# Kernel tuning notes

Measured on AMD Instinct MI355X. Metric: run time of the kernel, lower is better.

## Reference

```python
import jax, jax.numpy as jnp
import numpy as np

DIM = 2048
N_HEADS = 32
HEAD_DIM = DIM // N_HEADS
D_FF = 4 * DIM
EPS = 1e-5


def layernorm(x, g, b):
    mu = jnp.mean(x, axis=-1, keepdims=True)
    var = jnp.mean(jnp.square(x - mu), axis=-1, keepdims=True)
    return (x - mu) * jax.lax.rsqrt(var + EPS) * g + b


def setup_inputs() -> dict:
    key = jax.random.key(0)
    ks = jax.random.split(key, 12)
    s = 0.02
    # Linear weights stored as [in, out] (y = x @ W + b), equivalent math to torch's x @ W.T
    return {
        "x": jax.random.normal(ks[0], (2, 2048, DIM), jnp.float32),
        "w_qkv": jax.random.normal(ks[1], (DIM, 3 * DIM), jnp.float32) * s,
        "b_qkv": jnp.zeros((3 * DIM,), jnp.float32),
        "w_o": jax.random.normal(ks[2], (DIM, DIM), jnp.float32) * s,
        "b_o": jnp.zeros((DIM,), jnp.float32),
        "g1": jnp.ones((DIM,), jnp.float32),
        "beta1": jnp.zeros((DIM,), jnp.float32),
        "w1": jax.random.normal(ks[3], (DIM, D_FF), jnp.float32) * s,
        "b1": jnp.zeros((D_FF,), jnp.float32),
        "w2": jax.random.normal(ks[4], (D_FF, DIM), jnp.float32) * s,
        "b2": jnp.zeros((DIM,), jnp.float32),
        "g2": jnp.ones((DIM,), jnp.float32),
        "beta2": jnp.zeros((DIM,), jnp.float32),
    }


def reference(x, w_qkv, b_qkv, w_o, b_o, g1, beta1, w1, b1, w2, b2, g2, beta2):
    B, T, _ = x.shape
    residual = x
    h = layernorm(x, g1, beta1)
    qkv = h @ w_qkv + b_qkv                      # [B,T,3*DIM]
    qkv = qkv.reshape(B, T, 3, N_HEADS, HEAD_DIM)
    qkv = jnp.transpose(qkv, (2, 0, 3, 1, 4))    # [3,B,H,T,D]
    q, k, v = qkv[0], qkv[1], qkv[2]
    scores = jnp.einsum("bhtd,bhsd->bhts", q, k) / np.sqrt(HEAD_DIM).astype(np.float32)
    attn = jax.nn.softmax(scores, axis=-1)       # full T x T (non-causal), as in source
    out = jnp.einsum("bhts,bhsd->bhtd", attn, v)
    out = jnp.transpose(out, (0, 2, 1, 3)).reshape(B, T, DIM)
    h = out @ w_o + b_o
    x = h + residual
    residual = x
    h = layernorm(x, g2, beta2)
    h = jax.nn.gelu(h @ w1 + b1, approximate=False)  # torch nn.GELU default = exact erf
    h = h @ w2 + b2
    return h + residual
```

## Files before the change

kernel.cpp:

```cpp
#include <hip/hip_runtime.h>
#include <hip/hip_bf16.h>

#define DIM  2048
#define DFF  8192
#define NH   32
#define HD   64
#define TT   2048
#define MM   4096

typedef __attribute__((ext_vector_type(4))) float f32x4;
typedef __attribute__((ext_vector_type(4))) unsigned int u32x4;
typedef __attribute__((ext_vector_type(2))) unsigned int u32x2;
typedef unsigned short ushort_t;

#define MFMA16(ACC, A, B) \
  asm volatile("v_mfma_f32_16x16x32_bf16 %0, %1, %2, %0" : "+v"(ACC) : "v"(A), "v"(B))
#define MFMA16A(ACC, A, B) \
  asm volatile("v_mfma_f32_16x16x32_bf16 %0, %1, %2, %0" : "+a"(ACC) : "v"(A), "v"(B))

#define GL16(GP, LP)                                                     \
  __builtin_amdgcn_global_load_lds(                                      \
      (const __attribute__((address_space(1))) void*)(GP),               \
      (__attribute__((address_space(3))) void*)(LP), 16, 0, 0)

#define VM(N) do{ asm volatile("s_waitcnt vmcnt(" #N ")");               \
                  __builtin_amdgcn_sched_barrier(0); }while(0)
#define NOOP  ((void)0)

template <int IMM>
__device__ __forceinline__ u32x4 dsr(unsigned a) {
  u32x4 d;
  asm volatile("ds_read_b128 %0, %1 offset:%2" : "=v"(d) : "v"(a), "i"(IMM));
  return d;
}

__device__ __forceinline__ unsigned int f2bu(float f) {
  union { __hip_bfloat16 h; unsigned short u; } c;
  c.h = __float2bfloat16(f);
  return (unsigned int)c.u;
}
__device__ __forceinline__ float fexp2(float x) {
  float r; asm("v_exp_f32 %0, %1" : "=v"(r) : "v"(x)); return r;
}
__device__ __forceinline__ unsigned cvtpk(float lo, float hi) {
  unsigned r; asm("v_cvt_pk_bf16_f32 %0, %1, %2" : "=v"(r) : "v"(lo), "v"(hi));
  return r;
}
__device__ __forceinline__ float fmax3(float a, float b, float c) {
  float r; asm("v_max3_f32 %0, %1, %2, %3" : "=v"(r) : "v"(a), "v"(b), "v"(c));
  return r;
}

__global__ __launch_bounds__(256)
void transpose_cvt(const float* __restrict__ in, __hip_bfloat16* __restrict__ out,
                   int R, int C) {
  __shared__ float tile[32][33];
  const int tx = threadIdx.x, ty = threadIdx.y;
  const int bx = blockIdx.x * 32, by = blockIdx.y * 32;
#pragma unroll
  for (int i = 0; i < 32; i += 8)
    tile[ty + i][tx] = in[(size_t)(by + ty + i) * C + bx + tx];
  __syncthreads();
#pragma unroll
  for (int i = 0; i < 32; i += 8)
    out[(size_t)(bx + ty + i) * R + by + tx] = __float2bfloat16(tile[tx][ty + i]);
}

__global__ __launch_bounds__(256)
void ln_kernel(const float* __restrict__ in, const float* __restrict__ gw,
               const float* __restrict__ bw, __hip_bfloat16* __restrict__ out) {
  const int row = blockIdx.x;
  const int t = threadIdx.x;
  const float* x = in + (size_t)row * DIM;
  const float4 v0 = ((const float4*)x)[t * 2];
  const float4 v1 = ((const float4*)x)[t * 2 + 1];
  float s  = v0.x + v0.y + v0.z + v0.w + v1.x + v1.y + v1.z + v1.w;
  float ss = v0.x*v0.x + v0.y*v0.y + v0.z*v0.z + v0.w*v0.w
           + v1.x*v1.x + v1.y*v1.y + v1.z*v1.z + v1.w*v1.w;
#pragma unroll
  for (int o = 32; o >= 1; o >>= 1) { s += __shfl_xor(s, o); ss += __shfl_xor(ss, o); }
  __shared__ float red[8];
  if ((t & 63) == 0) { red[t >> 6] = s; red[4 + (t >> 6)] = ss; }
  __syncthreads();
  s  = red[0] + red[1] + red[2] + red[3];
  ss = red[4] + red[5] + red[6] + red[7];
  const float mean = s * (1.0f / DIM);
  const float rstd = rsqrtf(ss * (1.0f / DIM) - mean * mean + 1e-5f);
  const float4 g0 = ((const float4*)gw)[t * 2], g1 = ((const float4*)gw)[t * 2 + 1];
  const float4 b0 = ((const float4*)bw)[t * 2], b1 = ((const float4*)bw)[t * 2 + 1];
  uint4 o;
  o.x = f2bu((v0.x - mean) * rstd * g0.x + b0.x) | (f2bu((v0.y - mean) * rstd * g0.y + b0.y) << 16);
  o.y = f2bu((v0.z - mean) * rstd * g0.z + b0.z) | (f2bu((v0.w - mean) * rstd * g0.w + b0.w) << 16);
  o.z = f2bu((v1.x - mean) * rstd * g1.x + b1.x) | (f2bu((v1.y - mean) * rstd * g1.y + b1.y) << 16);
  o.w = f2bu((v1.z - mean) * rstd * g1.z + b1.z) | (f2bu((v1.w - mean) * rstd * g1.w + b1.w) << 16);
  *(uint4*)((char*)out + ((size_t)row * DIM + t * 8) * 2) = o;
}

template <int EPI>
__global__ __launch_bounds__(512, 2)
void gemm256(const __hip_bfloat16* __restrict__ Abf, const __hip_bfloat16* __restrict__ Btbf,
             const float* __restrict__ bias, const float* __restrict__ res,
             void* __restrict__ o0, void* __restrict__ o1, void* __restrict__ o2,
             int M, int N, int K, int nkt) {
  __shared__ ushort_t lds[2][2][16384];
  const int tid = threadIdx.x;
  const int l = tid & 63, w = tid >> 6;
  const int wm = w >> 2, wn = w & 3;
  const int g = l >> 4, q15 = l & 15;

  const int nby = M >> 8;
  const int nwg = (N >> 8) * nby;
  int id = blockIdx.x;
  {
    const int qq = nwg >> 3, rr = nwg & 7;
    const int xcd = id & 7, pos = id >> 3;
    id = (xcd < rr ? xcd * (qq + 1) : rr * (qq + 1) + (xcd - rr) * qq) + pos;
  }
  const int bm = (id % nby) << 8;
  const int bn = (id / nby) << 8;
  const int k0 = (EPI == 4) ? (int)blockIdx.y * (nkt << 6) : 0;

  const ushort_t* Au = (const ushort_t*)Abf;
  const ushort_t* Bu = (const ushort_t*)Btbf;
  const int sr = tid >> 3;
  const int sc = (((tid & 7) ^ (sr & 7)) << 3);
  const ushort_t* aBase = Au + (size_t)(bm + sr) * K + (k0 + sc);
  const ushort_t* bBase = Bu + (size_t)(bn + sr) * K + (k0 + sc);
  const int dOff = (w << 9) + (l << 3);

#define SA(BUF, GRP, KT_)                                                \
  GL16(aBase + (size_t)((GRP) << 6) * K + ((KT_) << 6),                  \
       &lds[BUF][0][((GRP) << 12) + dOff])
#define SB(BUF, GRP, KT_)                                                \
  GL16(bBase + (size_t)((GRP) << 6) * K + ((KT_) << 6),                  \
       &lds[BUF][1][((GRP) << 12) + dOff])

  const unsigned lbase =
      (unsigned)(size_t)(__attribute__((address_space(3))) ushort_t*)&lds[0][0][0];
  const int x7 = q15 & 7;
  const unsigned laneA = (unsigned)(q15 * 128);
  const unsigned c0 = (unsigned)((g ^ x7) * 16);
  const unsigned c1 = (unsigned)(((4 | g) ^ x7) * 16);
  const unsigned aAk0b0 = lbase + wm * 8192 + laneA + c0;
  const unsigned aAk1b0 = lbase + wm * 8192 + laneA + c1;
  const unsigned aAk0b1 = aAk0b0 + 65536;
  const unsigned aAk1b1 = aAk1b0 + 65536;
  const unsigned aBk0b0 = lbase + 32768 + wn * 8192 + laneA + c0;
  const unsigned aBk1b0 = lbase + 32768 + wn * 8192 + laneA + c1;
  const unsigned aBk0b1 = aBk0b0 + 65536;
  const unsigned aBk1b1 = aBk1b0 + 65536;

#define AOFFC(M) (((M) & 4) * 4096 + ((M) & 3) * 2048)
#define RDA(BUF, M0, M1) do{                                             \
    af[0][0] = dsr<AOFFC(M0)>(aAk0b##BUF);                               \
    af[0][1] = dsr<AOFFC(M0)>(aAk1b##BUF);                               \
    af[1][0] = dsr<AOFFC(M1)>(aAk0b##BUF);                               \
    af[1][1] = dsr<AOFFC(M1)>(aAk1b##BUF); }while(0)
#define RDB(BUF) do{                                                     \
    bf[0][0] = dsr<0>(aBk0b##BUF);    bf[0][1] = dsr<0>(aBk1b##BUF);     \
    bf[1][0] = dsr<2048>(aBk0b##BUF); bf[1][1] = dsr<2048>(aBk1b##BUF);  \
    bf[2][0] = dsr<4096>(aBk0b##BUF); bf[2][1] = dsr<4096>(aBk1b##BUF);  \
    bf[3][0] = dsr<6144>(aBk0b##BUF); bf[3][1] = dsr<6144>(aBk1b##BUF); }while(0)

#define LGK0 do{ asm volatile("s_waitcnt lgkmcnt(0)");                   \
                 __builtin_amdgcn_sched_barrier(0); }while(0)

#define CLUSTER(R0, R1) do{                                              \
    __builtin_amdgcn_s_setprio(1);                                       \
    MFMA16A(acc[R0][0], af[0][0], bf[0][0]);                             \
    MFMA16A(acc[R0][1], af[0][0], bf[1][0]);                             \
    MFMA16A(acc[R0][2], af[0][0], bf[2][0]);                             \
    MFMA16A(acc[R0][3], af[0][0], bf[3][0]);                             \
    MFMA16A(acc[R1][0], af[1][0], bf[0][0]);                             \
    MFMA16A(acc[R1][1], af[1][0], bf[1][0]);                             \
    MFMA16A(acc[R1][2], af[1][0], bf[2][0]);                             \
    MFMA16A(acc[R1][3], af[1][0], bf[3][0]);                             \
    MFMA16A(acc[R0][0], af[0][1], bf[0][1]);                             \
    MFMA16A(acc[R0][1], af[0][1], bf[1][1]);                             \
    MFMA16A(acc[R0][2], af[0][1], bf[2][1]);                             \
    MFMA16A(acc[R0][3], af[0][1], bf[3][1]);                             \
    MFMA16A(acc[R1][0], af[1][1], bf[0][1]);                             \
    MFMA16A(acc[R1][1], af[1][1], bf[1][1]);                             \
    MFMA16A(acc[R1][2], af[1][1], bf[2][1]);                             \
    MFMA16A(acc[R1][3], af[1][1], bf[3][1]);                             \
    __builtin_amdgcn_s_setprio(0); }while(0)

#define HALF(BUF, OBUF, ktA23, PFA, ktN, PFN, W1C, W3C)                  \
  do {                                                                   \
    if (PFA) { SA(OBUF, 2, ktA23); SA(OBUF, 3, ktA23); }                 \
    RDB(BUF); RDA(BUF, 0, 1);                                            \
    __builtin_amdgcn_s_barrier();                                        \
    LGK0; CLUSTER(0, 1);                                                 \
    __builtin_amdgcn_s_barrier();                                        \
    if (PFN) { SB(BUF, 0, ktN); SB(BUF, 1, ktN); }                       \
    RDA(BUF, 2, 3);                                                      \
    __builtin_amdgcn_s_barrier();                                        \
    LGK0; CLUSTER(2, 3);                                                 \
    W1C;                                                                 \
    __builtin_amdgcn_s_barrier();                                        \
    if (PFN) { SB(BUF, 2, ktN); SB(BUF, 3, ktN); }                       \
    RDA(BUF, 4, 5);                                                      \
    __builtin_amdgcn_s_barrier();                                        \
    LGK0; CLUSTER(4, 5);                                                 \
    __builtin_amdgcn_s_barrier();                                        \
    if (PFN) { SA(BUF, 0, ktN); SA(BUF, 1, ktN); }                       \
    RDA(BUF, 6, 7);                                                      \
    __builtin_amdgcn_s_barrier();                                        \
    LGK0; CLUSTER(6, 7);                                                 \
    W3C;                                                                 \
    __builtin_amdgcn_s_barrier();                                        \
  } while (0)

  f32x4 acc[8][4];
#pragma unroll
  for (int a = 0; a < 8; ++a)
#pragma unroll
    for (int b = 0; b < 4; ++b) acc[a][b] = (f32x4)0.0f;

  u32x4 bf[4][2], af[2][2];

  SB(0, 0, 0); SB(0, 1, 0); SB(0, 2, 0); SB(0, 3, 0);
  SA(0, 0, 0); SA(0, 1, 0); SA(0, 2, 0); SA(0, 3, 0);
  SB(1, 0, 1); SB(1, 1, 1); SB(1, 2, 1); SB(1, 3, 1);
  SA(1, 0, 1); SA(1, 1, 1);
  VM(8);
  __builtin_amdgcn_s_barrier();

  int kt = 0;
  for (; kt + 3 < nkt; kt += 2) {
    HALF(0, 1, kt + 1, true, kt + 2, true, VM(10), VM(8));
    HALF(1, 0, kt + 2, true, kt + 3, true, VM(10), VM(8));
  }
  HALF(0, 1, kt + 1, true,  kt + 2, false, VM(8), VM(2));
  HALF(1, 0, kt + 2, false, kt + 3, false, VM(0), NOOP);

#pragma unroll
  for (int m = 0; m < 8; ++m) {
    const int row0 = bm + ((m & 4) << 5) + (wm << 6) + ((m & 3) << 4) + (g << 2);
#pragma unroll
    for (int n = 0; n < 4; ++n) {
      const int col = bn + (wn << 6) + (n << 4) + q15;
      float bv = 0.0f;
      if constexpr (EPI != 4) bv = bias[col];
#pragma unroll
      for (int i = 0; i < 4; ++i) {
        const int mrow = row0 + i;
        float v = acc[m][n][i] + bv;
        if constexpr (EPI == 0) {
          const int sel = col >> 11, hd = col & 2047, h = hd >> 6, d = hd & 63;
          const int b = mrow >> 11, t = mrow & 2047;
          if (sel == 0) {
            ((__hip_bfloat16*)o0)[((size_t)(b * NH + h) * TT + t) * HD + d] =
                __float2bfloat16(v * 0.18033688011112042f);
          } else if (sel == 1) {
            ((__hip_bfloat16*)o1)[((size_t)(b * NH + h) * TT + t) * HD + d] =
                __float2bfloat16(v);
          } else {
            ((__hip_bfloat16*)o2)[((size_t)(b * NH + h) * HD + d) * TT + t] =
                __float2bfloat16(v);
          }
        } else if constexpr (EPI == 2) {
          ((__hip_bfloat16*)o0)[(size_t)mrow * N + col] =
              __float2bfloat16(0.5f * v * (1.0f + erff(v * 0.70710678118654752f)));
        } else {
          ((float*)(blockIdx.y ? o1 : o0))[(size_t)mrow * N + col] = v;
        }
      }
    }
  }
#undef SA
#undef SB
#undef RDA
#undef RDB
#undef HALF
#undef CLUSTER
#undef LGK0
#undef AOFFC
}

__global__ __launch_bounds__(256)
void combine2(const float* __restrict__ p0, const float* __restrict__ p1,
              const float* __restrict__ bias, const float* __restrict__ res,
              float* __restrict__ out) {
  const size_t i = ((size_t)blockIdx.x * 256 + threadIdx.x) << 2;
  const float4 a = *(const float4*)(p0 + i);
  const float4 b = *(const float4*)(p1 + i);
  const float4 r = *(const float4*)(res + i);
  const float4 bi = *(const float4*)(bias + (i & (DIM - 1)));
  float4 o;
  o.x = a.x + b.x + r.x + bi.x;
  o.y = a.y + b.y + r.y + bi.y;
  o.z = a.z + b.z + r.z + bi.z;
  o.w = a.w + b.w + r.w + bi.w;
  *(float4*)(out + i) = o;
}

template <int EPI>
__global__ __launch_bounds__(256)
void gemm_bt(const __hip_bfloat16* __restrict__ A, const __hip_bfloat16* __restrict__ Bt,
             const float* __restrict__ bias, const float* __restrict__ res,
             void* __restrict__ o0, int M, int N, int K) {
  __shared__ __hip_bfloat16 As[128 * 32];
  __shared__ __hip_bfloat16 Bs[128 * 32];
  const int tid = threadIdx.x;
  const int l = tid & 63, w = tid >> 6;
  const int wr = w >> 1, wc = w & 1;
  const int g = l >> 4, q15 = l & 15;
  const int bm = blockIdx.y * 128, bn = blockIdx.x * 128;

  f32x4 acc[4][4];
#pragma unroll
  for (int a = 0; a < 4; ++a)
#pragma unroll
    for (int b = 0; b < 4; ++b) acc[a][b] = (f32x4)0.0f;

  const __hip_bfloat16* aSrc = A  + (size_t)(bm + (tid >> 2)) * K + (tid & 3) * 8;
  const __hip_bfloat16* bSrc = Bt + (size_t)(bn + (tid >> 2)) * K + (tid & 3) * 8;
  __hip_bfloat16* aDst = As + tid * 8;
  __hip_bfloat16* bDst = Bs + tid * 8;
  const size_t rowStep = (size_t)64 * K;

  for (int kt = 0; kt < K; kt += 32) {
    GL16(aSrc + kt,            aDst);
    GL16(aSrc + rowStep + kt,  aDst + 2048);
    GL16(bSrc + kt,            bDst);
    GL16(bSrc + rowStep + kt,  bDst + 2048);
    __syncthreads();
    u32x4 af[4], bf[4];
#pragma unroll
    for (int rb = 0; rb < 4; ++rb)
      af[rb] = *(const u32x4*)(As + (wr * 64 + rb * 16 + q15) * 32 + g * 8);
#pragma unroll
    for (int cb = 0; cb < 4; ++cb)
      bf[cb] = *(const u32x4*)(Bs + (wc * 64 + cb * 16 + q15) * 32 + g * 8);
#pragma unroll
    for (int rb = 0; rb < 4; ++rb)
#pragma unroll
      for (int cb = 0; cb < 4; ++cb) MFMA16(acc[rb][cb], af[rb], bf[cb]);
    __syncthreads();
  }

#pragma unroll
  for (int rb = 0; rb < 4; ++rb) {
    const int row0 = bm + wr * 64 + rb * 16 + g * 4;
#pragma unroll
    for (int cb = 0; cb < 4; ++cb) {
      const int col = bn + wc * 64 + cb * 16 + q15;
      const float bv = bias[col];
#pragma unroll
      for (int i = 0; i < 4; ++i) {
        const int m = row0 + i;
        float v = acc[rb][cb][i] + bv;
        ((float*)o0)[(size_t)m * N + col] = v + res[(size_t)m * N + col];
      }
    }
  }
}

__global__ __launch_bounds__(256)
void attn_kernel(const __hip_bfloat16* __restrict__ Q, const __hip_bfloat16* __restrict__ Kx,
                 const __hip_bfloat16* __restrict__ Vt, __hip_bfloat16* __restrict__ out) {
  __shared__ unsigned int Plds[4][2048];
  const int tid = threadIdx.x;
  const int l = tid & 63, w = tid >> 6;
  const int g = l >> 4, q15 = l & 15;
  const int bh = blockIdx.x >> 3;
  const int q0 = (blockIdx.x & 7) * 256 + w * 64;
  const __hip_bfloat16* Qb = Q  + (size_t)bh * TT * HD;
  const __hip_bfloat16* Kb = Kx + (size_t)bh * TT * HD;
  const __hip_bfloat16* Vb = Vt + (size_t)bh * HD * TT;
  unsigned int* Pw = Plds[w];

  u32x4 qf[4][2];
#pragma unroll
  for (int rb = 0; rb < 4; ++rb)
#pragma unroll
    for (int ks = 0; ks < 2; ++ks)
      qf[rb][ks] = *(const u32x4*)(Qb + (size_t)(q0 + rb * 16 + q15) * HD + ks * 32 + g * 8);

  f32x4 acc[4][4];
#pragma unroll
  for (int a = 0; a < 4; ++a)
#pragma unroll
    for (int b = 0; b < 4; ++b) acc[a][b] = (f32x4)0.0f;
  float mstat[4] = {-3e38f, -3e38f, -3e38f, -3e38f};
  float lstat[4] = {0.f, 0.f, 0.f, 0.f};

  u32x4 kf[2][4];
#pragma unroll
  for (int cb = 0; cb < 4; ++cb)
#pragma unroll
    for (int ks = 0; ks < 2; ++ks)
      kf[ks][cb] = *(const u32x4*)(Kb + (size_t)(cb * 16 + q15) * HD + ks * 32 + g * 8);

  for (int s0 = 0; s0 < TT; s0 += 64) {
    f32x4 st[4][4];
#pragma unroll
    for (int a = 0; a < 4; ++a)
#pragma unroll
      for (int b = 0; b < 4; ++b) st[a][b] = (f32x4)0.0f;
    __builtin_amdgcn_s_setprio(1);
#pragma unroll
    for (int ks = 0; ks < 2; ++ks)
#pragma unroll
      for (int cb = 0; cb < 4; ++cb)
#pragma unroll
        for (int rb = 0; rb < 4; ++rb) MFMA16(st[cb][rb], kf[ks][cb], qf[rb][ks]);
    __builtin_amdgcn_s_setprio(0);
    if (s0 + 64 < TT) {
#pragma unroll
      for (int cb = 0; cb < 4; ++cb)
#pragma unroll
        for (int ks = 0; ks < 2; ++ks)
          kf[ks][cb] = *(const u32x4*)(Kb + (size_t)(s0 + 64 + cb * 16 + q15) * HD + ks * 32 + g * 8);
    }
#pragma unroll
    for (int rb = 0; rb < 4; ++rb) {
      float a0 = fmax3(st[0][rb][0], st[0][rb][1], st[0][rb][2]);
      float a1 = fmax3(st[0][rb][3], st[1][rb][0], st[1][rb][1]);
      float a2 = fmax3(st[1][rb][2], st[1][rb][3], st[2][rb][0]);
      float a3 = fmax3(st[2][rb][1], st[2][rb][2], st[2][rb][3]);
      float a4 = fmax3(st[3][rb][0], st[3][rb][1], st[3][rb][2]);
      float pm = fmax3(fmax3(a0, a1, a2), a3, fmax3(a4, st[3][rb][3], a0));
      pm = fmaxf(pm, __shfl_xor(pm, 16));
      pm = fmaxf(pm, __shfl_xor(pm, 32));
      if (!__all(pm <= mstat[rb] + 8.0f)) {
        const float mnew = fmaxf(mstat[rb], pm);
        const float corr = fexp2(mstat[rb] - mnew);
        mstat[rb] = mnew;
        lstat[rb] *= corr;
#pragma unroll
        for (int db = 0; db < 4; ++db)
#pragma unroll
          for (int i = 0; i < 4; ++i) acc[db][rb][i] *= corr;
      }
      const float mcur = mstat[rb];
      float rs = 0.f;
      const int row = rb * 16 + q15;
      const int rx = row & 7;
#pragma unroll
      for (int cb = 0; cb < 4; ++cb) {
        const float p0 = fexp2(st[cb][rb][0] - mcur);
        const float p1 = fexp2(st[cb][rb][1] - mcur);
        const float p2 = fexp2(st[cb][rb][2] - mcur);
        const float p3 = fexp2(st[cb][rb][3] - mcur);
        rs += (p0 + p1) + (p2 + p3);
        const int seg = (cb * 2 + (g >> 1)) ^ rx;
        u32x2 pk = {cvtpk(p0, p1), cvtpk(p2, p3)};
        *(u32x2*)(Pw + row * 32 + seg * 4 + (g & 1) * 2) = pk;
      }
      rs += __shfl_xor(rs, 16);
      rs += __shfl_xor(rs, 32);
      lstat[rb] += rs;
    }
    u32x4 vf[2][4];
#pragma unroll
    for (int ks2 = 0; ks2 < 2; ++ks2)
#pragma unroll
      for (int db = 0; db < 4; ++db)
        vf[ks2][db] = *(const u32x4*)(Vb + (size_t)(db * 16 + q15) * TT + s0 + ks2 * 32 + g * 8);
    u32x4 pf[2][4];
#pragma unroll
    for (int ks2 = 0; ks2 < 2; ++ks2)
#pragma unroll
      for (int rb = 0; rb < 4; ++rb) {
        const int row = rb * 16 + q15;
        const int seg = (ks2 * 4 + g) ^ (row & 7);
        pf[ks2][rb] = *(const u32x4*)(Pw + row * 32 + seg * 4);
      }
    __builtin_amdgcn_s_setprio(1);
#pragma unroll
    for (int ks2 = 0; ks2 < 2; ++ks2)
#pragma unroll
      for (int db = 0; db < 4; ++db)
#pragma unroll
        for (int rb = 0; rb < 4; ++rb) MFMA16(acc[db][rb], vf[ks2][db], pf[ks2][rb]);
    __builtin_amdgcn_s_setprio(0);
  }
  const int b = bh >> 5, hh = bh & 31;
#pragma unroll
  for (int rb = 0; rb < 4; ++rb) {
    const float inv = 1.0f / lstat[rb];
    const size_t trow = (size_t)(b * TT + q0 + rb * 16 + q15);
#pragma unroll
    for (int db = 0; db < 4; ++db) {
      u32x2 pk = {cvtpk(acc[db][rb][0] * inv, acc[db][rb][1] * inv),
                  cvtpk(acc[db][rb][2] * inv, acc[db][rb][3] * inv)};
      *(u32x2*)(out + trow * DIM + hh * 64 + db * 16 + g * 4) = pk;
    }
  }
}

extern "C" void kernel_launch(void* const* d_in, const int* in_sizes, int n_in,
                              void* d_out, int out_size, void* d_ws, size_t ws_size,
                              hipStream_t stream) {
  (void)in_sizes; (void)n_in; (void)out_size; (void)ws_size;
  const float* x     = (const float*)d_in[0];
  const float* w_qkv = (const float*)d_in[1];
  const float* b_qkv = (const float*)d_in[2];
  const float* w_o   = (const float*)d_in[3];
  const float* b_o   = (const float*)d_in[4];
  const float* g1    = (const float*)d_in[5];
  const float* be1   = (const float*)d_in[6];
  const float* w1    = (const float*)d_in[7];
  const float* b1    = (const float*)d_in[8];
  const float* w2    = (const float*)d_in[9];
  const float* b2    = (const float*)d_in[10];
  const float* g2    = (const float*)d_in[11];
  const float* be2   = (const float*)d_in[12];

  char* ws = (char*)d_ws;
  size_t off = 0;
  auto alloc = [&](size_t bytes) {
    void* p = ws + off;
    off += (bytes + 255) & ~(size_t)255;
    return p;
  };
  __hip_bfloat16* WqkvT = (__hip_bfloat16*)alloc((size_t)6144 * 2048 * 2);
  __hip_bfloat16* WoT   = (__hip_bfloat16*)alloc((size_t)2048 * 2048 * 2);
  __hip_bfloat16* W1T   = (__hip_bfloat16*)alloc((size_t)8192 * 2048 * 2);
  __hip_bfloat16* W2T   = (__hip_bfloat16*)alloc((size_t)2048 * 8192 * 2);
  __hip_bfloat16* hbuf  = (__hip_bfloat16*)alloc((size_t)MM * DIM * 2);
  float*          xres  = (float*)alloc((size_t)MM * DIM * 4);
  __hip_bfloat16* Qb    = (__hip_bfloat16*)alloc((size_t)MM * DIM * 2);
  __hip_bfloat16* Kb    = (__hip_bfloat16*)alloc((size_t)MM * DIM * 2);
  __hip_bfloat16* Vtb   = (__hip_bfloat16*)alloc((size_t)MM * DIM * 2);
  __hip_bfloat16* attno = (__hip_bfloat16*)alloc((size_t)MM * DIM * 2);
  __hip_bfloat16* f1    = Qb;
  float* p0 = (float*)ws;
  float* p1 = (float*)(ws + (size_t)MM * DIM * 4);

  const dim3 tb(32, 8);
  transpose_cvt<<<dim3(6144 / 32, 2048 / 32), tb, 0, stream>>>(w_qkv, WqkvT, 2048, 6144);
  transpose_cvt<<<dim3(2048 / 32, 2048 / 32), tb, 0, stream>>>(w_o, WoT, 2048, 2048);
  transpose_cvt<<<dim3(8192 / 32, 2048 / 32), tb, 0, stream>>>(w1, W1T, 2048, 8192);
  transpose_cvt<<<dim3(2048 / 32, 8192 / 32), tb, 0, stream>>>(w2, W2T, 8192, 2048);

  ln_kernel<<<MM, 256, 0, stream>>>(x, g1, be1, hbuf);
  gemm256<0><<<dim3((6144 / 256) * (MM / 256)), 512, 0, stream>>>(
      hbuf, WqkvT, b_qkv, nullptr, Qb, Kb, Vtb, MM, 6144, 2048, 32);
  attn_kernel<<<512, 256, 0, stream>>>(Qb, Kb, Vtb, attno);
  gemm_bt<1><<<dim3(2048 / 128, MM / 128), 256, 0, stream>>>(
      attno, WoT, b_o, x, xres, MM, 2048, 2048);
  ln_kernel<<<MM, 256, 0, stream>>>(xres, g2, be2, hbuf);
  gemm256<2><<<dim3((8192 / 256) * (MM / 256)), 512, 0, stream>>>(
      hbuf, W1T, b1, nullptr, f1, nullptr, nullptr, MM, 8192, 2048, 32);
  gemm256<4><<<dim3((2048 / 256) * (MM / 256), 2), 512, 0, stream>>>(
      f1, W2T, nullptr, nullptr, p0, p1, nullptr, MM, 2048, 8192, 64);
  combine2<<<(MM * DIM) / 1024, 256, 0, stream>>>(p0, p1, b2, xres, (float*)d_out);
}
```

Measured before the change: 717.3 us.

## Store split-K partials in bf16 and run QKV projection on simple 128x128 GEMM

The two split-K partial outputs of the FFN down-projection are now written as bf16 instead of fp32, which halves the bytes written and reread by the combine kernel. The combine kernel now handles 8 elements per thread and converts the bf16 partials before summing. Separately, the QKV projection with its head-split epilogue moves from the pipelined 256-tile GEMM to the simpler 128x128 gemm_bt kernel, which now takes three output pointers. Rounding the partial sums to bf16 costs accuracy, and the simpler GEMM has no software pipelining, so the QKV projection may run slower.

After: 698.7 us. 1.03x faster.

```diff
diff --git a/kernel.cpp b/kernel.cpp
--- a/kernel.cpp
+++ b/kernel.cpp
@@ -246,9 +246,115 @@
       for (int i = 0; i < 4; ++i) {
         const int mrow = row0 + i;
         float v = acc[m][n][i] + bv;
+        if constexpr (EPI == 2) {
+          ((__hip_bfloat16*)o0)[(size_t)mrow * N + col] =
+              __float2bfloat16(0.5f * v * (1.0f + erff(v * 0.70710678118654752f)));
+        } else {
+          ((__hip_bfloat16*)(blockIdx.y ? o1 : o0))[(size_t)mrow * N + col] =
+              __float2bfloat16(v);
+        }
+      }
+    }
+  }
+#undef SA
+#undef SB
+#undef RDA
+#undef RDB
+#undef HALF
+#undef CLUSTER
+#undef LGK0
+#undef AOFFC
+}
+
+__global__ __launch_bounds__(256)
+void combine2(const __hip_bfloat16* __restrict__ p0, const __hip_bfloat16* __restrict__ p1,
+              const float* __restrict__ bias, const float* __restrict__ res,
+              float* __restrict__ out) {
+  const size_t i = ((size_t)blockIdx.x * 256 + threadIdx.x) << 3;
+  const uint4 a = *(const uint4*)(p0 + i);
+  const uint4 b = *(const uint4*)(p1 + i);
+  const float4 r0 = *(const float4*)(res + i);
+  const float4 r1 = *(const float4*)(res + i + 4);
+  const float4 bi0 = *(const float4*)(bias + (i & (DIM - 1)));
+  const float4 bi1 = *(const float4*)(bias + ((i + 4) & (DIM - 1)));
+  union { unsigned u; struct { unsigned short lo, hi; } s; } ua, ub;
+  float4 o0, o1;
+  ua.u = a.x; ub.u = b.x;
+  o0.x = (float)*(__hip_bfloat16*)&ua.s.lo + (float)*(__hip_bfloat16*)&ub.s.lo + r0.x + bi0.x;
+  o0.y = (float)*(__hip_bfloat16*)&ua.s.hi + (float)*(__hip_bfloat16*)&ub.s.hi + r0.y + bi0.y;
+  ua.u = a.y; ub.u = b.y;
+  o0.z = (float)*(__hip_bfloat16*)&ua.s.lo + (float)*(__hip_bfloat16*)&ub.s.lo + r0.z + bi0.z;
+  o0.w = (float)*(__hip_bfloat16*)&ua.s.hi + (float)*(__hip_bfloat16*)&ub.s.hi + r0.w + bi0.w;
+  ua.u = a.z; ub.u = b.z;
+  o1.x = (float)*(__hip_bfloat16*)&ua.s.lo + (float)*(__hip_bfloat16*)&ub.s.lo + r1.x + bi1.x;
+  o1.y = (float)*(__hip_bfloat16*)&ua.s.hi + (float)*(__hip_bfloat16*)&ub.s.hi + r1.y + bi1.y;
+  ua.u = a.w; ub.u = b.w;
+  o1.z = (float)*(__hip_bfloat16*)&ua.s.lo + (float)*(__hip_bfloat16*)&ub.s.lo + r1.z + bi1.z;
+  o1.w = (float)*(__hip_bfloat16*)&ua.s.hi + (float)*(__hip_bfloat16*)&ub.s.hi + r1.w + bi1.w;
+  *(float4*)(out + i) = o0;
+  *(float4*)(out + i + 4) = o1;
+}
+
+template <int EPI>
+__global__ __launch_bounds__(256)
+void gemm_bt(const __hip_bfloat16* __restrict__ A, const __hip_bfloat16* __restrict__ Bt,
+             const float* __restrict__ bias, const float* __restrict__ res,
+             void* __restrict__ o0, void* __restrict__ o1, void* __restrict__ o2,
+             int M, int N, int K) {
+  __shared__ __hip_bfloat16 As[128 * 32];
+  __shared__ __hip_bfloat16 Bs[128 * 32];
+  const int tid = threadIdx.x;
+  const int l = tid & 63, w = tid >> 6;
+  const int wr = w >> 1, wc = w & 1;
+  const int g = l >> 4, q15 = l & 15;
+  const int bm = blockIdx.y * 128, bn = blockIdx.x * 128;
+
+  f32x4 acc[4][4];
+#pragma unroll
+  for (int a = 0; a < 4; ++a)
+#pragma unroll
+    for (int b = 0; b < 4; ++b) acc[a][b] = (f32x4)0.0f;
+
+  const __hip_bfloat16* aSrc = A  + (size_t)(bm + (tid >> 2)) * K + (tid & 3) * 8;
+  const __hip_bfloat16* bSrc = Bt + (size_t)(bn + (tid >> 2)) * K + (tid & 3) * 8;
+  __hip_bfloat16* aDst = As + tid * 8;
+  __hip_bfloat16* bDst = Bs + tid * 8;
+  const size_t rowStep = (size_t)64 * K;
+
+  for (int kt = 0; kt < K; kt += 32) {
+    GL16(aSrc + kt,            aDst);
+    GL16(aSrc + rowStep + kt,  aDst + 2048);
+    GL16(bSrc + kt,            bDst);
+    GL16(bSrc + rowStep + kt,  bDst + 2048);
+    __syncthreads();
+    u32x4 af[4], bf[4];
+#pragma unroll
+    for (int rb = 0; rb < 4; ++rb)
+      af[rb] = *(const u32x4*)(As + (wr * 64 + rb * 16 + q15) * 32 + g * 8);
+#pragma unroll
+    for (int cb = 0; cb < 4; ++cb)
+      bf[cb] = *(const u32x4*)(Bs + (wc * 64 + cb * 16 + q15) * 32 + g * 8);
+#pragma unroll
+    for (int rb = 0; rb < 4; ++rb)
+#pragma unroll
+      for (int cb = 0; cb < 4; ++cb) MFMA16(acc[rb][cb], af[rb], bf[cb]);
+    __syncthreads();
+  }
+
+#pragma unroll
+  for (int rb = 0; rb < 4; ++rb) {
+    const int row0 = bm + wr * 64 + rb * 16 + g * 4;
+#pragma unroll
+    for (int cb = 0; cb < 4; ++cb) {
+      const int col = bn + wc * 64 + cb * 16 + q15;
+      const float bv = bias[col];
+#pragma unroll
+      for (int i = 0; i < 4; ++i) {
+        const int m = row0 + i;
+        float v = acc[rb][cb][i] + bv;
         if constexpr (EPI == 0) {
           const int sel = col >> 11, hd = col & 2047, h = hd >> 6, d = hd & 63;
-          const int b = mrow >> 11, t = mrow & 2047;
+          const int b = m >> 11, t = m & 2047;
           if (sel == 0) {
             ((__hip_bfloat16*)o0)[((size_t)(b * NH + h) * TT + t) * HD + d] =
                 __float2bfloat16(v * 0.18033688011112042f);
@@ -259,99 +365,9 @@
             ((__hip_bfloat16*)o2)[((size_t)(b * NH + h) * HD + d) * TT + t] =
                 __float2bfloat16(v);
           }
-        } else if constexpr (EPI == 2) {
-          ((__hip_bfloat16*)o0)[(size_t)mrow * N + col] =
-              __float2bfloat16(0.5f * v * (1.0f + erff(v * 0.70710678118654752f)));
         } else {
-          ((float*)(blockIdx.y ? o1 : o0))[(size_t)mrow * N + col] = v;
+          ((float*)o0)[(size_t)m * N + col] = v + res[(size_t)m * N + col];
         }
-      }
-    }
-  }
-#undef SA
-#undef SB
-#undef RDA
-#undef RDB
-#undef HALF
-#undef CLUSTER
-#undef LGK0
-#undef AOFFC
-}
-
-__global__ __launch_bounds__(256)
-void combine2(const float* __restrict__ p0, const float* __restrict__ p1,
-              const float* __restrict__ bias, const float* __restrict__ res,
-              float* __restrict__ out) {
-  const size_t i = ((size_t)blockIdx.x * 256 + threadIdx.x) << 2;
-  const float4 a = *(const float4*)(p0 + i);
-  const float4 b = *(const float4*)(p1 + i);
-  const float4 r = *(const float4*)(res + i);
-  const float4 bi = *(const float4*)(bias + (i & (DIM - 1)));
-  float4 o;
-  o.x = a.x + b.x + r.x + bi.x;
-  o.y = a.y + b.y + r.y + bi.y;
-  o.z = a.z + b.z + r.z + bi.z;
-  o.w = a.w + b.w + r.w + bi.w;
-  *(float4*)(out + i) = o;
-}
-
-template <int EPI>
-__global__ __launch_bounds__(256)
-void gemm_bt(const __hip_bfloat16* __restrict__ A, const __hip_bfloat16* __restrict__ Bt,
-             const float* __restrict__ bias, const float* __restrict__ res,
-             void* __restrict__ o0, int M, int N, int K) {
-  __shared__ __hip_bfloat16 As[128 * 32];
-  __shared__ __hip_bfloat16 Bs[128 * 32];
-  const int tid = threadIdx.x;
-  const int l = tid & 63, w = tid >> 6;
-  const int wr = w >> 1, wc = w & 1;
-  const int g = l >> 4, q15 = l & 15;
-  const int bm = blockIdx.y * 128, bn = blockIdx.x * 128;
-
-  f32x4 acc[4][4];
-#pragma unroll
-  for (int a = 0; a < 4; ++a)
-#pragma unroll
-    for (int b = 0; b < 4; ++b) acc[a][b] = (f32x4)0.0f;
-
-  const __hip_bfloat16* aSrc = A  + (size_t)(bm + (tid >> 2)) * K + (tid & 3) * 8;
-  const __hip_bfloat16* bSrc = Bt + (size_t)(bn + (tid >> 2)) * K + (tid & 3) * 8;
-  __hip_bfloat16* aDst = As + tid * 8;
-  __hip_bfloat16* bDst = Bs + tid * 8;
-  const size_t rowStep = (size_t)64 * K;
-
-  for (int kt = 0; kt < K; kt += 32) {
-    GL16(aSrc + kt,            aDst);
-    GL16(aSrc + rowStep + kt,  aDst + 2048);
-    GL16(bSrc + kt,            bDst);
-    GL16(bSrc + rowStep + kt,  bDst + 2048);
-    __syncthreads();
-    u32x4 af[4], bf[4];
-#pragma unroll
-    for (int rb = 0; rb < 4; ++rb)
-      af[rb] = *(const u32x4*)(As + (wr * 64 + rb * 16 + q15) * 32 + g * 8);
-#pragma unroll
-    for (int cb = 0; cb < 4; ++cb)
-      bf[cb] = *(const u32x4*)(Bs + (wc * 64 + cb * 16 + q15) * 32 + g * 8);
-#pragma unroll
-    for (int rb = 0; rb < 4; ++rb)
-#pragma unroll
-      for (int cb = 0; cb < 4; ++cb) MFMA16(acc[rb][cb], af[rb], bf[cb]);
-    __syncthreads();
-  }
-
-#pragma unroll
-  for (int rb = 0; rb < 4; ++rb) {
-    const int row0 = bm + wr * 64 + rb * 16 + g * 4;
-#pragma unroll
-    for (int cb = 0; cb < 4; ++cb) {
-      const int col = bn + wc * 64 + cb * 16 + q15;
-      const float bv = bias[col];
-#pragma unroll
-      for (int i = 0; i < 4; ++i) {
-        const int m = row0 + i;
-        float v = acc[rb][cb][i] + bv;
-        ((float*)o0)[(size_t)m * N + col] = v + res[(size_t)m * N + col];
       }
     }
   }
@@ -527,8 +543,8 @@
   __hip_bfloat16* Vtb   = (__hip_bfloat16*)alloc((size_t)MM * DIM * 2);
   __hip_bfloat16* attno = (__hip_bfloat16*)alloc((size_t)MM * DIM * 2);
   __hip_bfloat16* f1    = Qb;
-  float* p0 = (float*)ws;
-  float* p1 = (float*)(ws + (size_t)MM * DIM * 4);
+  __hip_bfloat16* p0 = (__hip_bfloat16*)ws;
+  __hip_bfloat16* p1 = (__hip_bfloat16*)(ws + (size_t)MM * DIM * 2);
 
   const dim3 tb(32, 8);
   transpose_cvt<<<dim3(6144 / 32, 2048 / 32), tb, 0, stream>>>(w_qkv, WqkvT, 2048, 6144);
@@ -537,15 +553,15 @@
   transpose_cvt<<<dim3(2048 / 32, 8192 / 32), tb, 0, stream>>>(w2, W2T, 8192, 2048);
 
   ln_kernel<<<MM, 256, 0, stream>>>(x, g1, be1, hbuf);
-  gemm256<0><<<dim3((6144 / 256) * (MM / 256)), 512, 0, stream>>>(
-      hbuf, WqkvT, b_qkv, nullptr, Qb, Kb, Vtb, MM, 6144, 2048, 32);
+  gemm_bt<0><<<dim3(6144 / 128, MM / 128), 256, 0, stream>>>(
+      hbuf, WqkvT, b_qkv, nullptr, Qb, Kb, Vtb, MM, 6144, 2048);
   attn_kernel<<<512, 256, 0, stream>>>(Qb, Kb, Vtb, attno);
   gemm_bt<1><<<dim3(2048 / 128, MM / 128), 256, 0, stream>>>(
-      attno, WoT, b_o, x, xres, MM, 2048, 2048);
+      attno, WoT, b_o, x, xres, nullptr, nullptr, MM, 2048, 2048);
   ln_kernel<<<MM, 256, 0, stream>>>(xres, g2, be2, hbuf);
   gemm256<2><<<dim3((8192 / 256) * (MM / 256)), 512, 0, stream>>>(
       hbuf, W1T, b1, nullptr, f1, nullptr, nullptr, MM, 8192, 2048, 32);
   gemm256<4><<<dim3((2048 / 256) * (MM / 256), 2), 512, 0, stream>>>(
       f1, W2T, nullptr, nullptr, p0, p1, nullptr, MM, 2048, 8192, 64);
-  combine2<<<(MM * DIM) / 1024, 256, 0, stream>>>(p0, p1, b2, xres, (float*)d_out);
-}
+  combine2<<<(MM * DIM) / 2048, 256, 0, stream>>>(p0, p1, b2, xres, (float*)d_out);
+}
```
